# Kernel tuning notes

Hardware: AMD Instinct MI355X
Metric: run time of the kernel (lower is better)

## Reference

```python
import jax, jax.numpy as jnp
import numpy as np

ENC_DIM, DEC_DIM, ATT_DIM = 2048, 512, 512
B, N = 256, 196


def setup_inputs() -> dict:
    key = jax.random.key(0)
    ks = jax.random.split(key, 8)
    s_enc = 1.0 / np.sqrt(ENC_DIM)
    s_dec = 1.0 / np.sqrt(DEC_DIM)
    s_full = 1.0 / np.sqrt(ATT_DIM)
    return {
        "encoder_out": jax.random.normal(ks[0], (B, N, ENC_DIM), jnp.float32),
        "hidden": jax.random.normal(ks[1], (B, DEC_DIM), jnp.float32),
        "W_enc": jax.random.uniform(ks[2], (ENC_DIM, ATT_DIM), jnp.float32, -s_enc, s_enc),
        "b_enc": jax.random.uniform(ks[3], (ATT_DIM,), jnp.float32, -s_enc, s_enc),
        "W_dec": jax.random.uniform(ks[4], (DEC_DIM, ATT_DIM), jnp.float32, -s_dec, s_dec),
        "b_dec": jax.random.uniform(ks[5], (ATT_DIM,), jnp.float32, -s_dec, s_dec),
        "W_full": jax.random.uniform(ks[6], (ATT_DIM, 1), jnp.float32, -s_full, s_full),
        "b_full": jax.random.uniform(ks[7], (1,), jnp.float32, -s_full, s_full),
    }


def reference(encoder_out, hidden, W_enc, b_enc, W_dec, b_dec, W_full, b_full):
    # enc proj: [B, N, A]; dec proj: [B, 1, A] broadcast over pixels
    att1 = jnp.einsum('bne,ea->bna', encoder_out, W_enc) + b_enc
    att2 = hidden @ W_dec + b_dec                       # [B, A]
    att = jax.nn.relu(att1 + att2[:, None, :])          # [B, N, A]
    scores = (jnp.einsum('bna,a->bn', att, W_full[:, 0]) + b_full[0])  # [B, N]
    alpha = jax.nn.softmax(scores, axis=1)              # softmax over pixels
    context = jnp.einsum('bne,bn->be', encoder_out, alpha)  # [B, E]
    return (context, alpha)
```

## Files before the change

kernel.cpp:

```cpp
#include <hip/hip_runtime.h>
#include <hip/hip_bf16.h>
#include <stdint.h>

#define ENC_DIM 2048
#define ATT_DIM 512
#define BATCH   256
#define NPIX    196
#define MROWS   (BATCH*NPIX)
#define CTX_OFF (BATCH*ENC_DIM)
#define KC      128
#define NCH     (ENC_DIM/KC)
#define MSUB    112
#define ABUF    (MSUB*KC*2)

typedef __attribute__((ext_vector_type(8))) short  short8;
typedef __attribute__((ext_vector_type(4))) float  f32x4;

__device__ __forceinline__ uint32_t f2bf(float x) {
    union { float f; uint32_t u; } v; v.f = x;
    return (v.u + 0x7FFFu + ((v.u >> 16) & 1u)) >> 16;
}

__global__ __launch_bounds__(256) void pack_wenc(const float* __restrict__ W,
                                                 unsigned short* __restrict__ Wp) {
    const int i  = blockIdx.x * 256 + threadIdx.x;
    const int n  = i & 511;
    const int kg = i >> 9;
    short8 v;
#pragma unroll
    for (int j = 0; j < 8; ++j)
        v[j] = (short)f2bf(W[(size_t)(kg * 8 + j) * 512 + n]);
    *(short8*)(Wp + (size_t)i * 8) = v;
}

__global__ __launch_bounds__(256) void att2_kernel(const float* __restrict__ hidden,
                                                   const float* __restrict__ Wdec,
                                                   const float* __restrict__ bdec,
                                                   const float* __restrict__ benc,
                                                   float* __restrict__ att2p) {
    __shared__ float h[512];
    const int b   = blockIdx.x;
    const int tid = threadIdx.x;
    h[tid]       = hidden[(size_t)b * 512 + tid];
    h[tid + 256] = hidden[(size_t)b * 512 + tid + 256];
    __syncthreads();
    float acc0 = bdec[tid]       + benc[tid];
    float acc1 = bdec[tid + 256] + benc[tid + 256];
#pragma unroll 4
    for (int k = 0; k < 512; ++k) {
        const float hk = h[k];
        acc0 = fmaf(hk, Wdec[(size_t)k * 512 + tid],       acc0);
        acc1 = fmaf(hk, Wdec[(size_t)k * 512 + tid + 256], acc1);
    }
    att2p[(size_t)b * 512 + tid]       = acc0;
    att2p[(size_t)b * 512 + tid + 256] = acc1;
}

__global__ __launch_bounds__(512, 2) void fused_kernel(const float* __restrict__ enc,
                                                       const unsigned short* __restrict__ Wp,
                                                       const float* __restrict__ att2p,
                                                       const float* __restrict__ Wfull,
                                                       float* __restrict__ out) {
    __shared__ __align__(16) unsigned char ldsA[2 * ABUF];
    __shared__ float lds_att2[ATT_DIM];
    __shared__ float lds_wf[ATT_DIM];
    __shared__ float lds_sc[224];
    __shared__ float salpha[NPIX];
    __shared__ float red[16];

    const int tid = threadIdx.x;
    const int w   = tid >> 6;
    const int l   = tid & 63;
    const int b   = blockIdx.x;

    lds_att2[tid] = att2p[(size_t)b * ATT_DIM + tid];
    lds_wf[tid]   = Wfull[tid];
    if (tid < 224) lds_sc[tid] = 0.0f;

    int boff[4];
#pragma unroll
    for (int nf = 0; nf < 4; ++nf)
        boff[nf] = (((l >> 4) * 512) + (w << 6) + (nf << 4) + (l & 15)) * 8;

    const int g  = tid & 31;
    const int rr = tid >> 5;
    const int aoffL0 = rr * 256 + (((g >> 1) ^ (rr & 7)) << 4) + ((g & 1) << 3);
    const int axk   = l & 7;
    const int afrow = (l & 15) << 8;

    for (int sub = 0; sub < 2; ++sub) {
        int rowOff[7];
#pragma unroll
        for (int i = 0; i < 7; ++i) {
            int grow = b * NPIX + sub * MSUB + rr + 16 * i;
            if (grow > MROWS - 1) grow = MROWS - 1;
            rowOff[i] = grow * ENC_DIM;
        }
        const float* aBase = enc + g * 4;

        f32x4 acc[7][4];
#pragma unroll
        for (int i = 0; i < 7; ++i)
#pragma unroll
            for (int j = 0; j < 4; ++j)
                acc[i][j] = (f32x4){0.f, 0.f, 0.f, 0.f};

        {
            f32x4 sA[7];
#pragma unroll
            for (int i = 0; i < 7; ++i) sA[i] = *(const f32x4*)(aBase + rowOff[i]);
#pragma unroll
            for (int i = 0; i < 7; ++i) {
                uint2 u;
                u.x = f2bf(sA[i][0]) | (f2bf(sA[i][1]) << 16);
                u.y = f2bf(sA[i][2]) | (f2bf(sA[i][3]) << 16);
                *(uint2*)(ldsA + aoffL0 + i * 4096) = u;
            }
        }
        __syncthreads();

        for (int c = 0; c < NCH; ++c) {
            const int p = c & 1;
            const unsigned char* ldsR = ldsA + p * ABUF;
            unsigned char*       ldsW = ldsA + (p ^ 1) * ABUF;
            const bool more = (c < NCH - 1);

            f32x4 sA[7];
            if (more) {
#pragma unroll
                for (int i = 0; i < 7; ++i)
                    sA[i] = *(const f32x4*)(aBase + rowOff[i] + (c + 1) * KC);
            }

            const unsigned short* bC = Wp + (size_t)c * 65536;
            short8 bf0[8], bf1[8];
#pragma unroll
            for (int s2 = 0; s2 < 2; ++s2)
#pragma unroll
                for (int nf = 0; nf < 4; ++nf)
                    bf0[s2 * 4 + nf] = *(const short8*)(bC + boff[nf] + s2 * 16384);

#define STEP(S, BARR, BASE)                                                        \
            {                                                                      \
                const int so = ((((S) * 4) + (l >> 4)) ^ axk) << 4;                \
                _Pragma("unroll")                                                  \
                for (int mf = 0; mf < 7; ++mf) {                                   \
                    short8 af = *(const short8*)(ldsR + afrow + so + mf * 4096);   \
                    _Pragma("unroll")                                              \
                    for (int nf = 0; nf < 4; ++nf)                                 \
                        acc[mf][nf] = __builtin_amdgcn_mfma_f32_16x16x32_bf16(     \
                            af, BARR[(BASE) + nf], acc[mf][nf], 0, 0, 0);          \
                }                                                                  \
            }

            STEP(0, bf0, 0)
#pragma unroll
            for (int s2 = 0; s2 < 2; ++s2)
#pragma unroll
                for (int nf = 0; nf < 4; ++nf)
                    bf1[s2 * 4 + nf] = *(const short8*)(bC + boff[nf] + (2 + s2) * 16384);
            STEP(1, bf0, 4)
            STEP(2, bf1, 0)
            STEP(3, bf1, 4)
#undef STEP

            if (more) {
#pragma unroll
                for (int i = 0; i < 7; ++i) {
                    uint2 u;
                    u.x = f2bf(sA[i][0]) | (f2bf(sA[i][1]) << 16);
                    u.y = f2bf(sA[i][2]) | (f2bf(sA[i][3]) << 16);
                    *(uint2*)(ldsW + aoffL0 + i * 4096) = u;
                }
            }
            __syncthreads();
        }

#pragma unroll
        for (int mf = 0; mf < 7; ++mf) {
#pragma unroll
            for (int reg = 0; reg < 4; ++reg) {
                const int row = sub * MSUB + mf * 16 + ((l >> 4) << 2) + reg;
                float sv = 0.0f;
#pragma unroll
                for (int nf = 0; nf < 4; ++nf) {
                    const int col = (w << 6) + (nf << 4) + (l & 15);
                    float v = acc[mf][nf][reg] + lds_att2[col];
                    v = fmaxf(v, 0.0f);
                    sv = fmaf(v, lds_wf[col], sv);
                }
                sv += __shfl_xor(sv, 8);
                sv += __shfl_xor(sv, 4);
                sv += __shfl_xor(sv, 2);
                sv += __shfl_xor(sv, 1);
                if ((l & 15) == 0 && row < NPIX) atomicAdd(&lds_sc[row], sv);
            }
        }
    }
    __syncthreads();

    const float sval = (tid < NPIX) ? lds_sc[tid] : -1e30f;
    float mx = sval;
#pragma unroll
    for (int m = 32; m >= 1; m >>= 1) mx = fmaxf(mx, __shfl_xor(mx, m));
    if (l == 0) red[w] = mx;
    __syncthreads();
    if (tid == 0) {
        float m2 = red[0];
#pragma unroll
        for (int i = 1; i < 8; ++i) m2 = fmaxf(m2, red[i]);
        red[8] = m2;
    }
    __syncthreads();
    const float bm = red[8];
    const float ex = (tid < NPIX) ? __expf(sval - bm) : 0.0f;
    float sm = ex;
#pragma unroll
    for (int m = 32; m >= 1; m >>= 1) sm += __shfl_xor(sm, m);
    if (l == 0) red[w] = sm;
    __syncthreads();
    if (tid == 0) {
        float s2 = 0.f;
#pragma unroll
        for (int i = 0; i < 8; ++i) s2 += red[i];
        red[9] = s2;
    }
    __syncthreads();
    const float inv = 1.0f / red[9];
    if (tid < NPIX) {
        const float av = ex * inv;
        salpha[tid] = av;
        out[CTX_OFF + (size_t)b * NPIX + tid] = av;
    }
    __syncthreads();

    const float* ep = enc + (size_t)b * NPIX * ENC_DIM + tid * 4;
    f32x4 a2 = (f32x4){0.f, 0.f, 0.f, 0.f};
#pragma unroll 4
    for (int n = 0; n < NPIX; ++n)
        a2 += salpha[n] * *(const f32x4*)(ep + (size_t)n * ENC_DIM);
    *(f32x4*)(out + (size_t)b * ENC_DIM + tid * 4) = a2;
}

extern "C" void kernel_launch(void* const* d_in, const int* in_sizes, int n_in,
                              void* d_out, int out_size, void* d_ws, size_t ws_size,
                              hipStream_t stream) {
    const float* enc    = (const float*)d_in[0];
    const float* hidden = (const float*)d_in[1];
    const float* Wenc   = (const float*)d_in[2];
    const float* benc   = (const float*)d_in[3];
    const float* Wdec   = (const float*)d_in[4];
    const float* bdec   = (const float*)d_in[5];
    const float* Wfull  = (const float*)d_in[6];
    float* out = (float*)d_out;

    unsigned short* Wp    = (unsigned short*)d_ws;
    float*          att2p = (float*)((char*)d_ws + (2u << 20));

    pack_wenc   <<<512, 256, 0, stream>>>(Wenc, Wp);
    att2_kernel <<<BATCH, 256, 0, stream>>>(hidden, Wdec, bdec, benc, att2p);
    fused_kernel<<<BATCH, 512, 0, stream>>>(enc, Wp, att2p, Wfull, out);
}
```

Baseline: 289.1 us.

## Warp-specialize fused kernel with dedicated producer waves for encoder staging

```diff
diff --git a/kernel.cpp b/kernel.cpp
--- a/kernel.cpp
+++ b/kernel.cpp
@@ -6,10 +6,9 @@
 #define ATT_DIM 512
 #define BATCH   256
 #define NPIX    196
-#define MROWS   (BATCH*NPIX)
 #define CTX_OFF (BATCH*ENC_DIM)
 #define KC      128
-#define NCH     (ENC_DIM/KC)
+#define NITER   32
 #define MSUB    112
 #define ABUF    (MSUB*KC*2)
 
@@ -56,12 +55,12 @@
     att2p[(size_t)b * 512 + tid + 256] = acc1;
 }
 
-__global__ __launch_bounds__(512, 2) void fused_kernel(const float* __restrict__ enc,
+__global__ __launch_bounds__(768, 3) void fused_kernel(const float* __restrict__ enc,
                                                        const unsigned short* __restrict__ Wp,
                                                        const float* __restrict__ att2p,
                                                        const float* __restrict__ Wfull,
                                                        float* __restrict__ out) {
-    __shared__ __align__(16) unsigned char ldsA[2 * ABUF];
+    __shared__ __align__(16) unsigned char ldsA[2][ABUF];
     __shared__ float lds_att2[ATT_DIM];
     __shared__ float lds_wf[ATT_DIM];
     __shared__ float lds_sc[224];
@@ -69,164 +68,163 @@
     __shared__ float red[16];
 
     const int tid = threadIdx.x;
-    const int w   = tid >> 6;
-    const int l   = tid & 63;
     const int b   = blockIdx.x;
-
-    lds_att2[tid] = att2p[(size_t)b * ATT_DIM + tid];
-    lds_wf[tid]   = Wfull[tid];
+    const bool isProd = (tid >= 512);
+
+    if (tid < 512) {
+        lds_att2[tid] = att2p[(size_t)b * ATT_DIM + tid];
+        lds_wf[tid]   = Wfull[tid];
+    }
     if (tid < 224) lds_sc[tid] = 0.0f;
 
+    const int w    = tid >> 6;
+    const int l    = tid & 63;
+    const int kq   = l >> 4;
+    const int key2 = ((l & 7) << 1) ^ ((l >> 3) & 1);
+    const int afrow = (l & 15) << 8;
     int boff[4];
 #pragma unroll
     for (int nf = 0; nf < 4; ++nf)
-        boff[nf] = (((l >> 4) * 512) + (w << 6) + (nf << 4) + (l & 15)) * 8;
-
-    const int g  = tid & 31;
-    const int rr = tid >> 5;
-    const int aoffL0 = rr * 256 + (((g >> 1) ^ (rr & 7)) << 4) + ((g & 1) << 3);
-    const int axk   = l & 7;
-    const int afrow = (l & 15) << 8;
-
-    for (int sub = 0; sub < 2; ++sub) {
-        int rowOff[7];
-#pragma unroll
-        for (int i = 0; i < 7; ++i) {
-            int grow = b * NPIX + sub * MSUB + rr + 16 * i;
-            if (grow > MROWS - 1) grow = MROWS - 1;
-            rowOff[i] = grow * ENC_DIM;
-        }
-        const float* aBase = enc + g * 4;
-
-        f32x4 acc[7][4];
-#pragma unroll
-        for (int i = 0; i < 7; ++i)
-#pragma unroll
-            for (int j = 0; j < 4; ++j)
-                acc[i][j] = (f32x4){0.f, 0.f, 0.f, 0.f};
-
-        {
-            f32x4 sA[7];
-#pragma unroll
-            for (int i = 0; i < 7; ++i) sA[i] = *(const f32x4*)(aBase + rowOff[i]);
-#pragma unroll
-            for (int i = 0; i < 7; ++i) {
-                uint2 u;
-                u.x = f2bf(sA[i][0]) | (f2bf(sA[i][1]) << 16);
-                u.y = f2bf(sA[i][2]) | (f2bf(sA[i][3]) << 16);
-                *(uint2*)(ldsA + aoffL0 + i * 4096) = u;
+        boff[nf] = ((kq * 512) + (w << 6) + (nf << 4) + (l & 15)) * 8;
+
+    const int  pt    = tid - 512;
+    const bool pact  = isProd && (pt < 224);
+    const int  prow  = pt >> 1;
+    const int  phalf = pt & 1;
+    const int  pkey  = ((prow & 7) << 1) ^ ((prow >> 3) & 1);
+    int woff[8];
+#pragma unroll
+    for (int j2 = 0; j2 < 8; ++j2)
+        woff[j2] = prow * 256 + (((phalf * 8 + j2) ^ pkey) << 4);
+    int pix1 = 112 + prow; if (pix1 > NPIX - 1) pix1 = NPIX - 1;
+    const float* pbase0 = enc + ((size_t)b * NPIX + prow) * ENC_DIM + phalf * 64;
+    const float* pbase1 = enc + ((size_t)b * NPIX + pix1) * ENC_DIM + phalf * 64;
+
+#define PRODUCE(J, DSTBUF)                                                     \
+    {                                                                          \
+        const float* src = (((J) >> 4) ? pbase1 : pbase0) + ((J) & 15) * KC;   \
+        f32x4 r[16];                                                           \
+        _Pragma("unroll")                                                      \
+        for (int t = 0; t < 16; ++t) r[t] = *(const f32x4*)(src + t * 4);      \
+        unsigned char* ldsW = ldsA[(DSTBUF)];                                  \
+        _Pragma("unroll")                                                      \
+        for (int j2 = 0; j2 < 8; ++j2) {                                       \
+            uint4 wv;                                                          \
+            wv.x = f2bf(r[2*j2][0])   | (f2bf(r[2*j2][1])   << 16);            \
+            wv.y = f2bf(r[2*j2][2])   | (f2bf(r[2*j2][3])   << 16);            \
+            wv.z = f2bf(r[2*j2+1][0]) | (f2bf(r[2*j2+1][1]) << 16);            \
+            wv.w = f2bf(r[2*j2+1][2]) | (f2bf(r[2*j2+1][3]) << 16);            \
+            *(uint4*)(ldsW + woff[j2]) = wv;                                   \
+        }                                                                      \
+    }
+
+    if (pact) PRODUCE(0, 0)
+    __syncthreads();
+
+    f32x4 acc[7][4];
+#pragma unroll
+    for (int i = 0; i < 7; ++i)
+#pragma unroll
+        for (int j = 0; j < 4; ++j)
+            acc[i][j] = (f32x4){0.f, 0.f, 0.f, 0.f};
+
+#define STEP(S, B)                                                             \
+    {                                                                          \
+        const int so = (((S) * 4 + kq) ^ key2) << 4;                           \
+        _Pragma("unroll")                                                      \
+        for (int mf = 0; mf < 7; ++mf) {                                       \
+            short8 af = *(const short8*)(ldsR + afrow + so + mf * 4096);       \
+            _Pragma("unroll")                                                  \
+            for (int nf = 0; nf < 4; ++nf)                                     \
+                acc[mf][nf] = __builtin_amdgcn_mfma_f32_16x16x32_bf16(         \
+                    af, B[nf], acc[mf][nf], 0, 0, 0);                          \
+        }                                                                      \
+    }
+
+#pragma unroll 1
+    for (int i = 0; i < NITER; ++i) {
+        const int p = i & 1;
+        if (!isProd) {
+            const unsigned char*  ldsR = ldsA[p];
+            const unsigned short* bC   = Wp + (size_t)(i & 15) * 65536;
+            short8 b0[4], b1[4], b2[4], b3[4];
+#pragma unroll
+            for (int nf = 0; nf < 4; ++nf) b0[nf] = *(const short8*)(bC + boff[nf]);
+#pragma unroll
+            for (int nf = 0; nf < 4; ++nf) b1[nf] = *(const short8*)(bC + boff[nf] + 16384);
+            STEP(0, b0)
+#pragma unroll
+            for (int nf = 0; nf < 4; ++nf) b2[nf] = *(const short8*)(bC + boff[nf] + 32768);
+            STEP(1, b1)
+#pragma unroll
+            for (int nf = 0; nf < 4; ++nf) b3[nf] = *(const short8*)(bC + boff[nf] + 49152);
+            STEP(2, b2)
+            STEP(3, b3)
+
+            if (i == 15 || i == 31) {
+                const int sub = i >> 4;
+#pragma unroll
+                for (int mf = 0; mf < 7; ++mf) {
+#pragma unroll
+                    for (int reg = 0; reg < 4; ++reg) {
+                        const int row = sub * MSUB + mf * 16 + ((l >> 4) << 2) + reg;
+                        float sv = 0.0f;
+#pragma unroll
+                        for (int nf = 0; nf < 4; ++nf) {
+                            const int col = (w << 6) + (nf << 4) + (l & 15);
+                            float v = acc[mf][nf][reg] + lds_att2[col];
+                            v = fmaxf(v, 0.0f);
+                            sv = fmaf(v, lds_wf[col], sv);
+                        }
+                        sv += __shfl_xor(sv, 8);
+                        sv += __shfl_xor(sv, 4);
+                        sv += __shfl_xor(sv, 2);
+                        sv += __shfl_xor(sv, 1);
+                        if ((l & 15) == 0 && row < NPIX) atomicAdd(&lds_sc[row], sv);
+                    }
+                }
+#pragma unroll
+                for (int mf = 0; mf < 7; ++mf)
+#pragma unroll
+                    for (int nf = 0; nf < 4; ++nf)
+                        acc[mf][nf] = (f32x4){0.f, 0.f, 0.f, 0.f};
             }
+        } else if (pact) {
+            if (i < NITER - 1) PRODUCE(i + 1, p ^ 1)
         }
         __syncthreads();
-
-        for (int c = 0; c < NCH; ++c) {
-            const int p = c & 1;
-            const unsigned char* ldsR = ldsA + p * ABUF;
-            unsigned char*       ldsW = ldsA + (p ^ 1) * ABUF;
-            const bool more = (c < NCH - 1);
-
-            f32x4 sA[7];
-            if (more) {
-#pragma unroll
-                for (int i = 0; i < 7; ++i)
-                    sA[i] = *(const f32x4*)(aBase + rowOff[i] + (c + 1) * KC);
-            }
-
-            const unsigned short* bC = Wp + (size_t)c * 65536;
-            short8 bf0[8], bf1[8];
-#pragma unroll
-            for (int s2 = 0; s2 < 2; ++s2)
-#pragma unroll
-                for (int nf = 0; nf < 4; ++nf)
-                    bf0[s2 * 4 + nf] = *(const short8*)(bC + boff[nf] + s2 * 16384);
-
-#define STEP(S, BARR, BASE)                                                        \
-            {                                                                      \
-                const int so = ((((S) * 4) + (l >> 4)) ^ axk) << 4;                \
-                _Pragma("unroll")                                                  \
-                for (int mf = 0; mf < 7; ++mf) {                                   \
-                    short8 af = *(const short8*)(ldsR + afrow + so + mf * 4096);   \
-                    _Pragma("unroll")                                              \
-                    for (int nf = 0; nf < 4; ++nf)                                 \
-                        acc[mf][nf] = __builtin_amdgcn_mfma_f32_16x16x32_bf16(     \
-                            af, BARR[(BASE) + nf], acc[mf][nf], 0, 0, 0);          \
-                }                                                                  \
-            }
-
-            STEP(0, bf0, 0)
-#pragma unroll
-            for (int s2 = 0; s2 < 2; ++s2)
-#pragma unroll
-                for (int nf = 0; nf < 4; ++nf)
-                    bf1[s2 * 4 + nf] = *(const short8*)(bC + boff[nf] + (2 + s2) * 16384);
-            STEP(1, bf0, 4)
-            STEP(2, bf1, 0)
-            STEP(3, bf1, 4)
+    }
 #undef STEP
-
-            if (more) {
-#pragma unroll
-                for (int i = 0; i < 7; ++i) {
-                    uint2 u;
-                    u.x = f2bf(sA[i][0]) | (f2bf(sA[i][1]) << 16);
-                    u.y = f2bf(sA[i][2]) | (f2bf(sA[i][3]) << 16);
-                    *(uint2*)(ldsW + aoffL0 + i * 4096) = u;
-                }
-            }
-            __syncthreads();
-        }
-
-#pragma unroll
-        for (int mf = 0; mf < 7; ++mf) {
-#pragma unroll
-            for (int reg = 0; reg < 4; ++reg) {
-                const int row = sub * MSUB + mf * 16 + ((l >> 4) << 2) + reg;
-                float sv = 0.0f;
-#pragma unroll
-                for (int nf = 0; nf < 4; ++nf) {
-                    const int col = (w << 6) + (nf << 4) + (l & 15);
-                    float v = acc[mf][nf][reg] + lds_att2[col];
-                    v = fmaxf(v, 0.0f);
-                    sv = fmaf(v, lds_wf[col], sv);
-                }
-                sv += __shfl_xor(sv, 8);
-                sv += __shfl_xor(sv, 4);
-                sv += __shfl_xor(sv, 2);
-                sv += __shfl_xor(sv, 1);
-                if ((l & 15) == 0 && row < NPIX) atomicAdd(&lds_sc[row], sv);
-            }
-        }
-    }
-    __syncthreads();
+#undef PRODUCE
 
     const float sval = (tid < NPIX) ? lds_sc[tid] : -1e30f;
     float mx = sval;
 #pragma unroll
     for (int m = 32; m >= 1; m >>= 1) mx = fmaxf(mx, __shfl_xor(mx, m));
-    if (l == 0) red[w] = mx;
+    if (l == 0) red[tid >> 6] = mx;
     __syncthreads();
     if (tid == 0) {
         float m2 = red[0];
 #pragma unroll
-        for (int i = 1; i < 8; ++i) m2 = fmaxf(m2, red[i]);
-        red[8] = m2;
-    }
-    __syncthreads();
-    const float bm = red[8];
+        for (int i = 1; i < 12; ++i) m2 = fmaxf(m2, red[i]);
+        red[12] = m2;
+    }
+    __syncthreads();
+    const float bm = red[12];
     const float ex = (tid < NPIX) ? __expf(sval - bm) : 0.0f;
     float sm = ex;
 #pragma unroll
     for (int m = 32; m >= 1; m >>= 1) sm += __shfl_xor(sm, m);
-    if (l == 0) red[w] = sm;
+    if (l == 0) red[tid >> 6] = sm;
     __syncthreads();
     if (tid == 0) {
         float s2 = 0.f;
 #pragma unroll
-        for (int i = 0; i < 8; ++i) s2 += red[i];
-        red[9] = s2;
-    }
-    __syncthreads();
-    const float inv = 1.0f / red[9];
+        for (int i = 0; i < 12; ++i) s2 += red[i];
+        red[13] = s2;
+    }
+    __syncthreads();
+    const float inv = 1.0f / red[13];
     if (tid < NPIX) {
         const float av = ex * inv;
         salpha[tid] = av;
@@ -234,12 +232,14 @@
     }
     __syncthreads();
 
-    const float* ep = enc + (size_t)b * NPIX * ENC_DIM + tid * 4;
-    f32x4 a2 = (f32x4){0.f, 0.f, 0.f, 0.f};
+    if (tid < 512) {
+        const float* ep = enc + (size_t)b * NPIX * ENC_DIM + tid * 4;
+        f32x4 a2 = (f32x4){0.f, 0.f, 0.f, 0.f};
 #pragma unroll 4
-    for (int n = 0; n < NPIX; ++n)
-        a2 += salpha[n] * *(const f32x4*)(ep + (size_t)n * ENC_DIM);
-    *(f32x4*)(out + (size_t)b * ENC_DIM + tid * 4) = a2;
+        for (int n = 0; n < NPIX; ++n)
+            a2 += salpha[n] * *(const f32x4*)(ep + (size_t)n * ENC_DIM);
+        *(f32x4*)(out + (size_t)b * ENC_DIM + tid * 4) = a2;
+    }
 }
 
 extern "C" void kernel_launch(void* const* d_in, const int* in_sizes, int n_in,
@@ -259,5 +259,5 @@
 
     pack_wenc   <<<512, 256, 0, stream>>>(Wenc, Wp);
     att2_kernel <<<BATCH, 256, 0, stream>>>(hidden, Wdec, bdec, benc, att2p);
-    fused_kernel<<<BATCH, 512, 0, stream>>>(enc, Wp, att2p, Wfull, out);
-}
+    fused_kernel<<<BATCH, 768, 0, stream>>>(enc, Wp, att2p, Wfull, out);
+}
```

Measured after the change: 346.1 us. 1.2x slower.
